# Kernel optimization log

Hardware: AMD Instinct MI355X
Metric: run time of the kernel (lower is better)

## Reference

```python
import jax, jax.numpy as jnp
import numpy as np

V, E, H, T, B = 30000, 300, 300, 22, 4096

def setup_inputs() -> dict:
    key = jax.random.key(0)
    ks = jax.random.split(key, 10)
    cap = jax.random.randint(ks[0], (B, T), 0, V)
    cap_len = jax.random.randint(ks[1], (B,), 1, T + 1)  # valid lengths in [1, T]
    embed = jax.random.uniform(ks[2], (V, E), jnp.float32, -0.1, 0.1)
    s_ih = 1.0 / np.sqrt(H)
    W_ih = jax.random.uniform(ks[3], (4 * H, E), jnp.float32, -s_ih, s_ih)
    W_hh = jax.random.uniform(ks[4], (4 * H, H), jnp.float32, -s_ih, s_ih)
    b_ih = jax.random.uniform(ks[5], (4 * H,), jnp.float32, -s_ih, s_ih)
    b_hh = jax.random.uniform(ks[6], (4 * H,), jnp.float32, -s_ih, s_ih)
    v_wn = jax.random.normal(ks[7], (2, H), jnp.float32) * 0.05
    g_wn = jnp.linalg.norm(v_wn, axis=1)  # torch weight_norm init: g = ||v||
    b_cls = jnp.zeros((2,), jnp.float32)
    return {"cap": cap, "cap_len": cap_len, "embed": embed, "W_ih": W_ih,
            "W_hh": W_hh, "b_ih": b_ih, "b_hh": b_hh, "v_wn": v_wn,
            "g_wn": g_wn, "b_cls": b_cls}

def reference(cap, cap_len, embed, W_ih, W_hh, b_ih, b_hh, v_wn, g_wn, b_cls):
    Bn, Tn = cap.shape
    emb = embed[cap]                      # [B,T,E] embedding gather
    h0 = jnp.zeros((Bn, H), emb.dtype)
    c0 = jnp.zeros((Bn, H), emb.dtype)

    def step(carry, x_t):                 # x_t: [B,E]
        h, c = carry
        gates = x_t @ W_ih.T + b_ih + h @ W_hh.T + b_hh  # [B,4H]
        i, f, g, o = jnp.split(gates, 4, axis=-1)
        i = jax.nn.sigmoid(i); f = jax.nn.sigmoid(f); o = jax.nn.sigmoid(o)
        c = f * c + i * jnp.tanh(g)
        h = o * jnp.tanh(c)
        return (h, c), h

    _, hs = jax.lax.scan(step, (h0, c0), jnp.swapaxes(emb, 0, 1))  # hs: [T,B,H]
    hs = jnp.swapaxes(hs, 0, 1)                                    # [B,T,H]
    last = hs[jnp.arange(Bn), cap_len - 1]                         # [B,H] length-indexed gather
    # weight-normed linear head (dropout is identity at eval)
    W = g_wn[:, None] * v_wn / jnp.linalg.norm(v_wn, axis=1, keepdims=True)
    return last @ W.T + b_cls                                      # [B,2]
```

## Files before the change

### kernel.cpp

```cpp
#include <hip/hip_runtime.h>
#include <hip/hip_fp16.h>


#define TT 22
#define STEPS 22
#define NB 19
#define NGRP 8
#define GROWS 512
#define NWG (NB * NGRP)
#define NTHR 1024
#define KTOT 20
#define BUFELT ((size_t)256 * KTOT * 512)
#define SROWS 27

typedef _Float16 f16;
typedef _Float16 f16x8 __attribute__((ext_vector_type(8)));
typedef float    f32x4 __attribute__((ext_vector_type(4)));

__device__ __forceinline__ float sigm(float x) { return 1.0f / (1.0f + __expf(-x)); }
__device__ __forceinline__ float tanh_f(float x) {
    float ax = fabsf(x);
    float e = __expf(-2.0f * ax);
    return copysignf((1.0f - e) / (1.0f + e), x);
}
__device__ __forceinline__ f16x8 pack8(float4 a, float4 b) {
    f16x8 v;
    v[0] = (f16)a.x; v[1] = (f16)a.y; v[2] = (f16)a.z; v[3] = (f16)a.w;
    v[4] = (f16)b.x; v[5] = (f16)b.y; v[6] = (f16)b.z; v[7] = (f16)b.w;
    return v;
}

__global__ __launch_bounds__(NTHR, 4)
void lstm_ws(const int* __restrict__ cap, const int* __restrict__ cap_len,
             const float* __restrict__ embed,
             const float* __restrict__ Wih, const float* __restrict__ Whh,
             const float* __restrict__ bih, const float* __restrict__ bhh,
             const float* __restrict__ v_wn, const float* __restrict__ g_wn,
             const float* __restrict__ b_cls,
             f16* __restrict__ bufs, int depth,
             unsigned* __restrict__ bar, float* __restrict__ out)
{
    __shared__ f16 Wl[80 * 512];
    __shared__ int capS[SROWS][TT];
    __shared__ float scaleS[2];
    __shared__ unsigned idsS[NB];

    const int tid = threadIdx.x;
    const int b   = blockIdx.x;
    const int grp = b & 7;
    const int nb  = b >> 3;
    const int mrow0 = grp * GROWS;
    const int wv = tid >> 6, ln = tid & 63, c = ln & 15, kg = ln >> 4;

    unsigned* flags = bar + grp * 1024;
    unsigned* ids   = bar + grp * 1024 + 768;

    if (tid == 0)
        (void)__hip_atomic_load(flags, __ATOMIC_ACQUIRE, __HIP_MEMORY_SCOPE_AGENT);
    unsigned xcc;
    asm volatile("s_getreg_b32 %0, hwreg(HW_REG_XCC_ID)" : "=s"(xcc));
    if (tid == 0)
        __hip_atomic_store(ids + nb, xcc + 1u, __ATOMIC_RELAXED,
                           __HIP_MEMORY_SCOPE_AGENT);

    auto slot = [&](int n) { return bufs + (size_t)(n % depth) * BUFELT; };

    for (int u = tid; u < 80 * 64; u += NTHR) {
        int f = u >> 6, l = u & 63;
        int g = f / KTOT, kt = f - g * KTOT;
        int cc = l & 15, kgg = l >> 4;
        int jh0 = nb * 16 + cc;
        int j = g * 300 + jh0;
        int kb = kt * 32 + kgg * 8;
        f16x8 v;
        #pragma unroll
        for (int i = 0; i < 8; ++i) {
            int kk = kb + i;
            float x = 0.f;
            if (jh0 < 300) {
                if (kk < 300)                   x = Wih[(size_t)j * 300 + kk];
                else if (kk >= 320 && kk < 620) x = Whh[(size_t)j * 300 + (kk - 320)];
            }
            v[i] = (f16)x;
        }
        *(f16x8*)&Wl[(size_t)f * 512 + l * 8] = v;
    }

    const int srow0 = nb * SROWS;
    const int nr = (GROWS - srow0) < SROWS ? (GROWS - srow0) : SROWS;
    for (int u = tid; u < SROWS * TT; u += NTHR) {
        int rl = u / TT, t = u - rl * TT;
        if (rl < nr) capS[rl][t] = cap[(size_t)(mrow0 + srow0 + rl) * TT + t];
    }
    if (tid < 2) {
        float s = 0.f;
        for (int k = 0; k < 300; ++k) { float v = v_wn[tid * 300 + k]; s += v * v; }
        scaleS[tid] = g_wn[tid] * rsqrtf(s);
    }
    __syncthreads();

    auto stage_x = [&](int t, f16* bufn) {
        for (int u = tid; u < nr * 40; u += NTHR) {
            int rl = u / 40, k8 = u - rl * 40;
            int grow = mrow0 + srow0 + rl;
            const float* er = embed + (size_t)capS[rl][t] * 300;
            int k0 = k8 * 8;
            f16x8 v;
            if (k0 < 296) {
                v = pack8(*(const float4*)(er + k0), *(const float4*)(er + k0 + 4));
            } else if (k0 == 296) {
                float4 a = *(const float4*)(er + 296);
                v[0] = (f16)a.x; v[1] = (f16)a.y; v[2] = (f16)a.z; v[3] = (f16)a.w;
                v[4] = v[5] = v[6] = v[7] = (f16)0.f;
            } else {
                #pragma unroll
                for (int i = 0; i < 8; ++i) v[i] = (f16)0.f;
            }
            size_t off = ((size_t)((grow >> 4) * KTOT + (k8 >> 2))) * 512
                         + (grow & 15) * 32 + (k8 & 3) * 8;
            *(f16x8*)(bufn + off) = v;
        }
    };

    auto arrive = [&](unsigned ph, bool rel) {
        __syncthreads();
        if (tid == 0) {
            if (rel)
                __hip_atomic_store(flags + nb * 32, ph, __ATOMIC_RELEASE,
                                   __HIP_MEMORY_SCOPE_AGENT);
            else
                __hip_atomic_store(flags + nb * 32, ph, __ATOMIC_RELAXED,
                                   __HIP_MEMORY_SCOPE_AGENT);
        }
    };
    auto wait = [&](unsigned ph, bool fen) {
        if (tid < NB) {
            while (__hip_atomic_load(flags + tid * 32, __ATOMIC_RELAXED,
                                     __HIP_MEMORY_SCOPE_AGENT) < ph)
                __builtin_amdgcn_s_sleep(1);
        }
        if (fen)
            __builtin_amdgcn_fence(__ATOMIC_ACQUIRE, "agent");
        __syncthreads();
    };

    size_t aoff[2];
    #pragma unroll
    for (int m = 0; m < 2; ++m)
        aoff[m] = (size_t)(((mrow0 >> 4) + wv * 2 + m) * KTOT) * 512
                  + c * 32 + kg * 8;
    int wbase[4];
    #pragma unroll
    for (int g = 0; g < 4; ++g) wbase[g] = g * KTOT * 512 + ln * 8;

    const int jh = nb * 16 + c;
    float bias[4];
    #pragma unroll
    for (int g = 0; g < 4; ++g) {
        float bv = 0.f;
        if (jh < 300) { int j = g * 300 + jh; bv = bih[j] + bhh[j]; }
        bias[g] = bv;
    }
    int lenr[2][4];
    #pragma unroll
    for (int m = 0; m < 2; ++m) {
        int rb = mrow0 + wv * 32 + m * 16 + kg * 4;
        #pragma unroll
        for (int rg = 0; rg < 4; ++rg) lenr[m][rg] = cap_len[rb + rg];
    }
    const int hkt  = (320 + jh) >> 5;
    const int hkgd = ((320 + jh) >> 3) & 3;
    const int hel  = jh & 7;

    float cst[2][4] = {};
    float hreg[2][4] = {};
    f32x4 acc[2][4];

    auto xpart = [&](const f16* bufc) {
        #pragma unroll
        for (int kt = 0; kt < 10; ++kt) {
            f16x8 av[2];
            #pragma unroll
            for (int m = 0; m < 2; ++m)
                av[m] = *(const f16x8*)(bufc + aoff[m] + kt * 512);
            #pragma unroll
            for (int g = 0; g < 4; ++g) {
                f16x8 bv = *(const f16x8*)&Wl[wbase[g] + kt * 512];
                #pragma unroll
                for (int m = 0; m < 2; ++m)
                    acc[m][g] = __builtin_amdgcn_mfma_f32_16x16x32_f16(av[m], bv, acc[m][g], 0, 0, 0);
            }
        }
    };
    auto hpart = [&](const f16* bufc) {
        #pragma unroll
        for (int kt = 10; kt < KTOT; ++kt) {
            f16x8 av[2];
            #pragma unroll
            for (int m = 0; m < 2; ++m)
                av[m] = *(const f16x8*)(bufc + aoff[m] + kt * 512);
            #pragma unroll
            for (int g = 0; g < 4; ++g) {
                f16x8 bv = *(const f16x8*)&Wl[wbase[g] + kt * 512];
                #pragma unroll
                for (int m = 0; m < 2; ++m)
                    acc[m][g] = __builtin_amdgcn_mfma_f32_16x16x32_f16(av[m], bv, acc[m][g], 0, 0, 0);
            }
        }
    };

    const bool ahead2 = (depth >= 3);
    stage_x(0, slot(0));
    if (ahead2) stage_x(1, slot(1));
    arrive(1, true);
    wait(1, true);

    if (tid < NB)
        idsS[tid] = __hip_atomic_load(ids + tid, __ATOMIC_RELAXED,
                                      __HIP_MEMORY_SCOPE_AGENT);
    __syncthreads();
    bool fastp = true;
    #pragma unroll 1
    for (int i = 1; i < NB; ++i) fastp = fastp && (idsS[i] == idsS[0]);

    #pragma unroll 1
    for (int t = 0; t < STEPS; ++t) {
        const f16* bufc = slot(t);
        #pragma unroll
        for (int m = 0; m < 2; ++m)
            #pragma unroll
            for (int g = 0; g < 4; ++g) {
                float bv = bias[g];
                f32x4 b4 = {bv, bv, bv, bv};
                acc[m][g] = b4;
            }

        bool reuse = (unsigned)(t + 1) >= (unsigned)depth;
        if (ahead2) {
            xpart(bufc);
            wait((unsigned)(t + 1), reuse);
        } else {
            wait((unsigned)(t + 1), reuse);
            xpart(bufc);
        }
        hpart(bufc);

        f16* bufn = slot(t + 1);
        #pragma unroll
        for (int m = 0; m < 2; ++m) {
            int rtile = (mrow0 >> 4) + wv * 2 + m;
            size_t hb = ((size_t)(rtile * KTOT + hkt)) * 512 + hkgd * 8 + hel;
            #pragma unroll
            for (int rg = 0; rg < 4; ++rg) {
                bool upd = (t < lenr[m][rg]);
                float iv = sigm(acc[m][0][rg]);
                float fv = sigm(acc[m][1][rg]);
                float gv = tanh_f(acc[m][2][rg]);
                float ov = sigm(acc[m][3][rg]);
                float cn = fv * cst[m][rg] + iv * gv;
                cn = upd ? cn : cst[m][rg];
                cst[m][rg] = cn;
                float hn = ov * tanh_f(cn);
                hreg[m][rg] = upd ? hn : hreg[m][rg];
                f16 hv = (jh < 300) ? (f16)hreg[m][rg] : (f16)0.f;
                bufn[hb + (size_t)(kg * 4 + rg) * 32] = hv;
            }
        }

        if (ahead2) { if (t + 2 < STEPS) stage_x(t + 2, slot(t + 2)); }
        else        { if (t + 1 < STEPS) stage_x(t + 1, slot(t + 1)); }
        arrive((unsigned)(t + 2), !fastp);
    }

    wait((unsigned)(STEPS + 1), true);

    const f16* hb = slot(STEPS);
    for (int u = tid; u < nr * 2; u += NTHR) {
        int rl = u >> 1, cls = u & 1;
        int grow = mrow0 + srow0 + rl;
        float sc = scaleS[cls];
        const float* vr = v_wn + cls * 300;
        size_t rbase = ((size_t)((grow >> 4) * KTOT)) * 512 + (grow & 15) * 32;
        float s = 0.f;
        #pragma unroll 4
        for (int k = 0; k < 300; ++k) {
            int k2 = 320 + k;
            size_t off = rbase + (size_t)(k2 >> 5) * 512 + ((k2 >> 3) & 3) * 8 + (k2 & 7);
            s += vr[k] * (float)hb[off];
        }
        out[(size_t)grow * 2 + cls] = sc * s + b_cls[cls];
    }
}

extern "C" void kernel_launch(void* const* d_in, const int* in_sizes, int n_in,
                              void* d_out, int out_size, void* d_ws, size_t ws_size,
                              hipStream_t stream) {
    const int*   cap     = (const int*)  d_in[0];
    const int*   cap_len = (const int*)  d_in[1];
    const float* embed   = (const float*)d_in[2];
    const float* W_ih    = (const float*)d_in[3];
    const float* W_hh    = (const float*)d_in[4];
    const float* b_ih    = (const float*)d_in[5];
    const float* b_hh    = (const float*)d_in[6];
    const float* v_wn    = (const float*)d_in[7];
    const float* g_wn    = (const float*)d_in[8];
    const float* b_cls   = (const float*)d_in[9];
    float* out = (float*)d_out;

    unsigned* bar = (unsigned*)d_ws;
    f16* bufs = (f16*)((char*)d_ws + 65536);
    size_t slot_bytes = BUFELT * sizeof(f16);
    int depth = (int)((ws_size > 65536 ? ws_size - 65536 : 0) / slot_bytes);
    if (depth > STEPS + 1) depth = STEPS + 1;
    if (depth < 2) depth = 2;

    hipMemsetAsync(bar, 0, 65536, stream);
    hipMemsetAsync(bufs, 0, slot_bytes, stream);

    lstm_ws<<<NWG, NTHR, 0, stream>>>(cap, cap_len, embed, W_ih, W_hh, b_ih, b_hh,
                                      v_wn, g_wn, b_cls, bufs, depth, bar, out);
}
```

Before: 413.3 us.

## Replace block-level barrier with per-wave flags and add deeper x staging

Each wave now publishes its own progress flag, and every wave polls all 304 flags of its group directly. This replaces the __syncthreads plus single-thread flag and poll scheme. The aim is to remove the intra-block barriers from the recurrent step's critical path. A third lookahead depth stages the input projection three steps ahead when the buffer depth allows it, with that staging issued after the arrive. The cost is more polling traffic per wave, and the relaxed-store path relies on s_waitcnt for visibility.

```diff
diff --git a/kernel.cpp b/kernel.cpp
--- a/kernel.cpp
+++ b/kernel.cpp
@@ -9,9 +9,11 @@
 #define GROWS 512
 #define NWG (NB * NGRP)
 #define NTHR 1024
+#define NWAVE 16
 #define KTOT 20
 #define BUFELT ((size_t)256 * KTOT * 512)
 #define SROWS 27
+#define NFLG (NB * NWAVE)
 
 typedef _Float16 f16;
 typedef _Float16 f16x8 __attribute__((ext_vector_type(8)));
@@ -43,7 +45,6 @@
     __shared__ f16 Wl[80 * 512];
     __shared__ int capS[SROWS][TT];
     __shared__ float scaleS[2];
-    __shared__ unsigned idsS[NB];
 
     const int tid = threadIdx.x;
     const int b   = blockIdx.x;
@@ -52,15 +53,16 @@
     const int mrow0 = grp * GROWS;
     const int wv = tid >> 6, ln = tid & 63, c = ln & 15, kg = ln >> 4;
 
-    unsigned* flags = bar + grp * 1024;
-    unsigned* ids   = bar + grp * 1024 + 768;
+    unsigned* fbase  = bar + grp * 512;
+    unsigned* myflag = fbase + nb * NWAVE + wv;
+    unsigned* ids    = bar + 4096;
 
     if (tid == 0)
-        (void)__hip_atomic_load(flags, __ATOMIC_ACQUIRE, __HIP_MEMORY_SCOPE_AGENT);
+        (void)__hip_atomic_load(fbase, __ATOMIC_ACQUIRE, __HIP_MEMORY_SCOPE_AGENT);
     unsigned xcc;
     asm volatile("s_getreg_b32 %0, hwreg(HW_REG_XCC_ID)" : "=s"(xcc));
     if (tid == 0)
-        __hip_atomic_store(ids + nb, xcc + 1u, __ATOMIC_RELAXED,
+        __hip_atomic_store(ids + grp * NB + nb, xcc + 1u, __ATOMIC_RELAXED,
                            __HIP_MEMORY_SCOPE_AGENT);
 
     auto slot = [&](int n) { return bufs + (size_t)(n % depth) * BUFELT; };
@@ -122,26 +124,37 @@
         }
     };
 
-    auto arrive = [&](unsigned ph, bool rel) {
-        __syncthreads();
-        if (tid == 0) {
-            if (rel)
-                __hip_atomic_store(flags + nb * 32, ph, __ATOMIC_RELEASE,
+    bool fastp = true;
+    auto arriveW = [&](unsigned ph, bool rel) {
+        if (rel) {
+            if (ln == 0)
+                __hip_atomic_store(myflag, ph, __ATOMIC_RELEASE,
                                    __HIP_MEMORY_SCOPE_AGENT);
-            else
-                __hip_atomic_store(flags + nb * 32, ph, __ATOMIC_RELAXED,
+        } else {
+            asm volatile("s_waitcnt vmcnt(0)" ::: "memory");
+            if (ln == 0)
+                __hip_atomic_store(myflag, ph, __ATOMIC_RELAXED,
                                    __HIP_MEMORY_SCOPE_AGENT);
         }
     };
-    auto wait = [&](unsigned ph, bool fen) {
-        if (tid < NB) {
-            while (__hip_atomic_load(flags + tid * 32, __ATOMIC_RELAXED,
-                                     __HIP_MEMORY_SCOPE_AGENT) < ph)
-                __builtin_amdgcn_s_sleep(1);
+    auto waitW = [&](unsigned ph, bool fen) {
+        for (;;) {
+            bool ok = true;
+            #pragma unroll
+            for (int r = 0; r < 5; ++r) {
+                int idx = ln + r * 64;
+                if (idx < NFLG) {
+                    unsigned v = __hip_atomic_load(fbase + idx, __ATOMIC_RELAXED,
+                                                   __HIP_MEMORY_SCOPE_AGENT);
+                    ok = ok && (v >= ph);
+                }
+            }
+            if (__all(ok)) break;
+            __builtin_amdgcn_s_sleep(1);
         }
         if (fen)
             __builtin_amdgcn_fence(__ATOMIC_ACQUIRE, "agent");
-        __syncthreads();
+        asm volatile("" ::: "memory");
     };
 
     size_t aoff[2];
@@ -209,19 +222,19 @@
         }
     };
 
-    const bool ahead2 = (depth >= 3);
+    const int ah = (depth >= 6) ? 3 : (depth >= 3 ? 2 : 1);
     stage_x(0, slot(0));
-    if (ahead2) stage_x(1, slot(1));
-    arrive(1, true);
-    wait(1, true);
-
-    if (tid < NB)
-        idsS[tid] = __hip_atomic_load(ids + tid, __ATOMIC_RELAXED,
-                                      __HIP_MEMORY_SCOPE_AGENT);
-    __syncthreads();
-    bool fastp = true;
-    #pragma unroll 1
-    for (int i = 1; i < NB; ++i) fastp = fastp && (idsS[i] == idsS[0]);
+    if (ah >= 2) stage_x(1, slot(1));
+    if (ah == 3) stage_x(2, slot(2));
+    arriveW(1, true);
+    waitW(1, false);
+
+    {
+        unsigned idv = __hip_atomic_load(ids + grp * NB + (ln < NB ? ln : 0),
+                                         __ATOMIC_RELAXED, __HIP_MEMORY_SCOPE_AGENT);
+        unsigned id0 = (unsigned)__shfl((int)idv, 0);
+        fastp = __all(idv == id0);
+    }
 
     #pragma unroll 1
     for (int t = 0; t < STEPS; ++t) {
@@ -236,11 +249,11 @@
             }
 
         bool reuse = (unsigned)(t + 1) >= (unsigned)depth;
-        if (ahead2) {
+        if (ah >= 2) {
             xpart(bufc);
-            wait((unsigned)(t + 1), reuse);
+            waitW((unsigned)(t + 1), reuse);
         } else {
-            wait((unsigned)(t + 1), reuse);
+            waitW((unsigned)(t + 1), reuse);
             xpart(bufc);
         }
         hpart(bufc);
@@ -267,12 +280,13 @@
             }
         }
 
-        if (ahead2) { if (t + 2 < STEPS) stage_x(t + 2, slot(t + 2)); }
-        else        { if (t + 1 < STEPS) stage_x(t + 1, slot(t + 1)); }
-        arrive((unsigned)(t + 2), !fastp);
-    }
-
-    wait((unsigned)(STEPS + 1), true);
+        if (ah == 2 && t + 2 < STEPS) stage_x(t + 2, slot(t + 2));
+        if (ah == 1 && t + 1 < STEPS) stage_x(t + 1, slot(t + 1));
+        arriveW((unsigned)(t + 2), !fastp);
+        if (ah == 3 && t + 3 < STEPS) stage_x(t + 3, slot(t + 3));
+    }
+
+    waitW((unsigned)(STEPS + 1), true);
 
     const f16* hb = slot(STEPS);
     for (int u = tid; u < nr * 2; u += NTHR) {
```

Result: slower. 443.5 us (+7.3%).

## Assign block roles per XCC and vectorize hidden-state stores via LDS transpose

Applied to the files above, without the earlier changes.

The kernel now launches extra blocks and assigns each one a group and index from a per-XCC atomic counter. This puts all 19 blocks of a recurrent group on the same XCC, and surplus blocks exit. Because the group shares one L2, the per-step flag stores become relaxed and the acquire fences on the fast path are dropped. That removes release/acquire cost from every one of the 22 sequential barrier steps. New hidden-state values are also transposed through a shared-memory tile so they can be written as 16-byte vectors instead of scalar f16 stores. The risk is that correctness now depends on the hardware spreading blocks so that each XCC hosts at least 19 of them, and on same-XCC coherence without release fences.

```diff
diff --git a/kernel.cpp b/kernel.cpp
--- a/kernel.cpp
+++ b/kernel.cpp
@@ -5,9 +5,7 @@
 #define TT 22
 #define STEPS 22
 #define NB 19
-#define NGRP 8
-#define GROWS 512
-#define NWG (NB * NGRP)
+#define NWG 248
 #define NTHR 1024
 #define KTOT 20
 #define BUFELT ((size_t)256 * KTOT * 512)
@@ -41,27 +39,32 @@
              unsigned* __restrict__ bar, float* __restrict__ out)
 {
     __shared__ f16 Wl[80 * 512];
+    __shared__ float ts[16][16][17];
     __shared__ int capS[SROWS][TT];
     __shared__ float scaleS[2];
-    __shared__ unsigned idsS[NB];
+    __shared__ int roleS;
 
     const int tid = threadIdx.x;
-    const int b   = blockIdx.x;
-    const int grp = b & 7;
-    const int nb  = b >> 3;
-    const int mrow0 = grp * GROWS;
     const int wv = tid >> 6, ln = tid & 63, c = ln & 15, kg = ln >> 4;
 
+    __builtin_amdgcn_fence(__ATOMIC_ACQUIRE, "agent");
+
+    unsigned* cnt = bar + 12288;
+    if (tid == 0) {
+        unsigned xcc;
+        asm volatile("s_getreg_b32 %0, hwreg(HW_REG_XCC_ID)" : "=s"(xcc));
+        unsigned s = __hip_atomic_fetch_add(cnt + xcc * 64, 1u,
+                                            __ATOMIC_RELAXED,
+                                            __HIP_MEMORY_SCOPE_AGENT);
+        roleS = (int)(xcc * 32 + s);
+    }
+    __syncthreads();
+    const int grp = roleS >> 5;
+    const int nb  = roleS & 31;
+    if (nb >= NB) return;
+
+    const int mrow0 = grp * 512;
     unsigned* flags = bar + grp * 1024;
-    unsigned* ids   = bar + grp * 1024 + 768;
-
-    if (tid == 0)
-        (void)__hip_atomic_load(flags, __ATOMIC_ACQUIRE, __HIP_MEMORY_SCOPE_AGENT);
-    unsigned xcc;
-    asm volatile("s_getreg_b32 %0, hwreg(HW_REG_XCC_ID)" : "=s"(xcc));
-    if (tid == 0)
-        __hip_atomic_store(ids + nb, xcc + 1u, __ATOMIC_RELAXED,
-                           __HIP_MEMORY_SCOPE_AGENT);
 
     auto slot = [&](int n) { return bufs + (size_t)(n % depth) * BUFELT; };
 
@@ -87,7 +90,7 @@
     }
 
     const int srow0 = nb * SROWS;
-    const int nr = (GROWS - srow0) < SROWS ? (GROWS - srow0) : SROWS;
+    const int nr = (512 - srow0) < SROWS ? (512 - srow0) : SROWS;
     for (int u = tid; u < SROWS * TT; u += NTHR) {
         int rl = u / TT, t = u - rl * TT;
         if (rl < nr) capS[rl][t] = cap[(size_t)(mrow0 + srow0 + rl) * TT + t];
@@ -122,16 +125,11 @@
         }
     };
 
-    auto arrive = [&](unsigned ph, bool rel) {
+    auto arrive = [&](unsigned ph) {
         __syncthreads();
-        if (tid == 0) {
-            if (rel)
-                __hip_atomic_store(flags + nb * 32, ph, __ATOMIC_RELEASE,
-                                   __HIP_MEMORY_SCOPE_AGENT);
-            else
-                __hip_atomic_store(flags + nb * 32, ph, __ATOMIC_RELAXED,
-                                   __HIP_MEMORY_SCOPE_AGENT);
-        }
+        if (tid == 0)
+            __hip_atomic_store(flags + nb * 32, ph, __ATOMIC_RELAXED,
+                               __HIP_MEMORY_SCOPE_AGENT);
     };
     auto wait = [&](unsigned ph, bool fen) {
         if (tid < NB) {
@@ -168,9 +166,8 @@
         #pragma unroll
         for (int rg = 0; rg < 4; ++rg) lenr[m][rg] = cap_len[rb + rg];
     }
-    const int hkt  = (320 + jh) >> 5;
-    const int hkgd = ((320 + jh) >> 3) & 3;
-    const int hel  = jh & 7;
+    const int hkt   = 10 + (nb >> 1);
+    const int kbase = (nb & 1) * 16;
 
     float cst[2][4] = {};
     float hreg[2][4] = {};
@@ -212,16 +209,8 @@
     const bool ahead2 = (depth >= 3);
     stage_x(0, slot(0));
     if (ahead2) stage_x(1, slot(1));
-    arrive(1, true);
-    wait(1, true);
-
-    if (tid < NB)
-        idsS[tid] = __hip_atomic_load(ids + tid, __ATOMIC_RELAXED,
-                                      __HIP_MEMORY_SCOPE_AGENT);
-    __syncthreads();
-    bool fastp = true;
-    #pragma unroll 1
-    for (int i = 1; i < NB; ++i) fastp = fastp && (idsS[i] == idsS[0]);
+    arrive(1);
+    wait(1, false);
 
     #pragma unroll 1
     for (int t = 0; t < STEPS; ++t) {
@@ -248,8 +237,6 @@
         f16* bufn = slot(t + 1);
         #pragma unroll
         for (int m = 0; m < 2; ++m) {
-            int rtile = (mrow0 >> 4) + wv * 2 + m;
-            size_t hb = ((size_t)(rtile * KTOT + hkt)) * 512 + hkgd * 8 + hel;
             #pragma unroll
             for (int rg = 0; rg < 4; ++rg) {
                 bool upd = (t < lenr[m][rg]);
@@ -262,14 +249,23 @@
                 cst[m][rg] = cn;
                 float hn = ov * tanh_f(cn);
                 hreg[m][rg] = upd ? hn : hreg[m][rg];
-                f16 hv = (jh < 300) ? (f16)hreg[m][rg] : (f16)0.f;
-                bufn[hb + (size_t)(kg * 4 + rg) * 32] = hv;
+                ts[wv][kg * 4 + rg][c] = (jh < 300) ? hreg[m][rg] : 0.f;
+            }
+            if (ln < 32) {
+                int r = ln >> 1, hf = ln & 1;
+                f16x8 v;
+                #pragma unroll
+                for (int i = 0; i < 8; ++i) v[i] = (f16)ts[wv][r][hf * 8 + i];
+                int rtile = (mrow0 >> 4) + wv * 2 + m;
+                size_t dst = ((size_t)(rtile * KTOT + hkt)) * 512
+                             + r * 32 + kbase + hf * 8;
+                *(f16x8*)(bufn + dst) = v;
             }
         }
 
         if (ahead2) { if (t + 2 < STEPS) stage_x(t + 2, slot(t + 2)); }
         else        { if (t + 1 < STEPS) stage_x(t + 1, slot(t + 1)); }
-        arrive((unsigned)(t + 2), !fastp);
+        arrive((unsigned)(t + 2));
     }
 
     wait((unsigned)(STEPS + 1), true);
@@ -285,7 +281,7 @@
         #pragma unroll 4
         for (int k = 0; k < 300; ++k) {
             int k2 = 320 + k;
-            size_t off = rbase + (size_t)(k2 >> 5) * 512 + ((k2 >> 3) & 3) * 8 + (k2 & 7);
+            size_t off = rbase + (size_t)(k2 >> 5) * 512 + (k2 & 31);
             s += vr[k] * (float)hb[off];
         }
         out[(size_t)grow * 2 + cls] = sc * s + b_cls[cls];
```

After: 422.9 us. 2.3% more time.
